# Kernel optimization log

Measured on AMD Instinct MI355X. Metric: run time of the kernel, lower is better.

Reference implementation:

```python
import jax, jax.numpy as jnp
import numpy as np

B, L, D, H, NL = 4, 2048, 512, 8, 2
HD = D // H  # 64
EPS = 1e-5


def _rotate_half(t):
    a, b = jnp.split(t, 2, axis=-1)
    return jnp.concatenate([-b, a], axis=-1)


def _ln(x, w, b):
    mu = jnp.mean(x, axis=-1, keepdims=True)
    var = jnp.mean((x - mu) ** 2, axis=-1, keepdims=True)
    return (x - mu) * jax.lax.rsqrt(var + EPS) * w + b


def setup_inputs() -> dict:
    key = jax.random.key(0)
    ks = jax.random.split(key, 8)
    x = jax.random.normal(ks[0], (B, L, D), dtype=jnp.float32)
    # 1D RoPE built per head_dim, tiled across heads -> [B, L, D]
    pos = jnp.arange(L, dtype=jnp.float32)
    inv_freq = 10000.0 ** (-2.0 * jnp.arange(HD, dtype=jnp.float32) / HD)
    theta = pos[:, None] * inv_freq[None, :]  # [L, HD]
    pos_cos = jnp.broadcast_to(jnp.tile(jnp.cos(theta), (1, H))[None], (B, L, D)).astype(jnp.float32)
    pos_sin = jnp.broadcast_to(jnp.tile(jnp.sin(theta), (1, H))[None], (B, L, D)).astype(jnp.float32)
    attn_mask = jnp.zeros((B, L), dtype=jnp.float32)  # all tokens valid
    s = 0.02
    Wq = s * jax.random.normal(ks[1], (NL, D, D), dtype=jnp.float32)
    Wk = s * jax.random.normal(ks[2], (NL, D, D), dtype=jnp.float32)
    Wv = s * jax.random.normal(ks[3], (NL, D, D), dtype=jnp.float32)
    Wo = s * jax.random.normal(ks[4], (NL, D, D), dtype=jnp.float32)
    W1 = s * jax.random.normal(ks[5], (NL, D, 2 * D), dtype=jnp.float32)
    W2 = s * jax.random.normal(ks[6], (NL, D, D), dtype=jnp.float32)
    ln1_w = jnp.ones((NL, D), jnp.float32); ln1_b = jnp.zeros((NL, D), jnp.float32)
    ln2_w = jnp.ones((NL, D), jnp.float32); ln2_b = jnp.zeros((NL, D), jnp.float32)
    lnf_w = jnp.ones((D,), jnp.float32); lnf_b = jnp.zeros((D,), jnp.float32)
    return dict(x=x, pos_cos=pos_cos, pos_sin=pos_sin, attn_mask=attn_mask,
                Wq=Wq, Wk=Wk, Wv=Wv, Wo=Wo, W1=W1, W2=W2,
                ln1_w=ln1_w, ln1_b=ln1_b, ln2_w=ln2_w, ln2_b=ln2_b,
                lnf_w=lnf_w, lnf_b=lnf_b)


def reference(x, pos_cos, pos_sin, attn_mask, Wq, Wk, Wv, Wo, W1, W2,
              ln1_w, ln1_b, ln2_w, ln2_b, lnf_w, lnf_b):
    # [B, H, L, HD]
    cos = pos_cos.reshape(B, L, H, HD).transpose(0, 2, 1, 3)
    sin = pos_sin.reshape(B, L, H, HD).transpose(0, 2, 1, 3)
    mask = attn_mask[:, None, None, :]  # [B,1,1,L]
    scale = 1.0 / np.float32(np.sqrt(HD))
    for i in range(NL):
        xn = _ln(x, ln1_w[i], ln1_b[i])
        q = (xn @ Wq[i]).reshape(B, L, H, HD).transpose(0, 2, 1, 3)
        k = (xn @ Wk[i]).reshape(B, L, H, HD).transpose(0, 2, 1, 3)
        v = (xn @ Wv[i]).reshape(B, L, H, HD).transpose(0, 2, 1, 3)
        q = q * cos + _rotate_half(q) * sin
        k = k * cos + _rotate_half(k) * sin
        scores = jnp.einsum('bhqd,bhkd->bhqk', q, k) * scale + mask
        probs = jax.nn.softmax(scores, axis=-1)
        ctx = jnp.einsum('bhqk,bhkd->bhqd', probs, v)
        ctx = ctx.transpose(0, 2, 1, 3).reshape(B, L, D)
        x = x + ctx @ Wo[i]
        xn = _ln(x, ln2_w[i], ln2_b[i])
        h = xn @ W1[i]
        x1, x2 = jnp.split(h, 2, axis=-1)
        x = x + (jax.nn.silu(x1) * x2) @ W2[i]
    return _ln(x, lnf_w, lnf_b)
```

## Files before the change

### kernel.cpp

```cpp
#include <hip/hip_runtime.h>

#define BB 4
#define LL 2048
#define DD 512
#define HH 8
#define NLAYER 2

typedef __attribute__((ext_vector_type(8))) short short8;
typedef __attribute__((ext_vector_type(4))) float floatx4;
typedef __attribute__((ext_vector_type(16))) float floatx16;

union U4S8 { uint4 u4; short8 s8; unsigned int u[4]; };

__device__ __forceinline__ unsigned short f2bf(float f) {
  unsigned int u = __float_as_uint(f);
  u += 0x7fffu + ((u >> 16) & 1u);
  return (unsigned short)(u >> 16);
}
__device__ __forceinline__ float bf2f(unsigned short s) {
  return __uint_as_float(((unsigned int)s) << 16);
}
__device__ __forceinline__ unsigned int pack_bf16(float a0, float a1) {
  unsigned int u0 = __float_as_uint(a0) + 0x8000u;
  unsigned int u1 = __float_as_uint(a1) + 0x8000u;
  return __builtin_amdgcn_perm(u1, u0, 0x07060302u);
}
__device__ __forceinline__ unsigned int pack_bf16_trunc(float a0, float a1) {
  return __builtin_amdgcn_perm(__float_as_uint(a1), __float_as_uint(a0), 0x07060302u);
}
__device__ __forceinline__ float fast_exp2(float x) {
#if __has_builtin(__builtin_amdgcn_exp2f)
  return __builtin_amdgcn_exp2f(x);
#else
  return exp2f(x);
#endif
}
__device__ __forceinline__ float fast_exp(float x) {
  return fast_exp2(x * 1.442695040888963f);
}

struct TJob { const float* src; unsigned short* dst; int C; int il; };
struct TJobs { TJob j[12]; };

__global__ __launch_bounds__(256) void transpose_all_kernel(TJobs jobs) {
  TJob jb = jobs.j[blockIdx.z];
  int c0 = blockIdx.x * 32;
  if (c0 >= jb.C) return;
  const int R = 512;
  __shared__ float t[32][33];
  int r0 = blockIdx.y * 32;
#pragma unroll
  for (int i = 0; i < 4; i++) {
    int idx = threadIdx.x + i * 256;
    t[idx >> 5][idx & 31] = jb.src[(size_t)(r0 + (idx >> 5)) * jb.C + c0 + (idx & 31)];
  }
  __syncthreads();
#pragma unroll
  for (int i = 0; i < 4; i++) {
    int idx = threadIdx.x + i * 256;
    int cc = idx >> 5, rr = idx & 31;
    int c = c0 + cc;
    int orow = jb.il ? ((c < 512) ? 2 * c : 2 * (c - 512) + 1) : c;
    jb.dst[(size_t)orow * R + r0 + rr] = f2bf(t[rr][cc]);
  }
}

__global__ __launch_bounds__(256) void ln_kernel(
    const float* __restrict__ x, const float* __restrict__ w, const float* __restrict__ b,
    unsigned short* __restrict__ outB, float* __restrict__ outF) {
  int row = blockIdx.x;
  const float* xr = x + (size_t)row * DD;
  int tid = threadIdx.x;
  float2 v = *(const float2*)(xr + tid * 2);
  float s = v.x + v.y;
  float ss = v.x * v.x + v.y * v.y;
#pragma unroll
  for (int off = 1; off < 64; off <<= 1) {
    s += __shfl_xor(s, off);
    ss += __shfl_xor(ss, off);
  }
  __shared__ float red[2][4];
  int wave = tid >> 6, lane = tid & 63;
  if (lane == 0) { red[0][wave] = s; red[1][wave] = ss; }
  __syncthreads();
  s = red[0][0] + red[0][1] + red[0][2] + red[0][3];
  ss = red[1][0] + red[1][1] + red[1][2] + red[1][3];
  float mu = s * (1.0f / DD);
  float var = ss * (1.0f / DD) - mu * mu;
  float inv = rsqrtf(var + 1e-5f);
#pragma unroll
  for (int j = 0; j < 2; j++) {
    int c = tid * 2 + j;
    float val = (((j == 0) ? v.x : v.y) - mu) * inv * w[c] + b[c];
    if (outB) outB[(size_t)row * DD + c] = f2bf(val);
    if (outF) outF[(size_t)row * DD + c] = val;
  }
}

__global__ __launch_bounds__(256) void gemm128_kernel(
    const unsigned short* __restrict__ A, const unsigned short* __restrict__ Bt,
    float* __restrict__ outF, unsigned short* __restrict__ outB,
    const float* __restrict__ res, int M, int N, int K,
    unsigned short* __restrict__ vtp) {
  __shared__ alignas(16) unsigned short As[128 * 32];
  __shared__ alignas(16) unsigned short Bs[128 * 32];
  const int tid = threadIdx.x;
  const int wave = tid >> 6, lane = tid & 63;
  const int l16 = lane & 15, quad = lane >> 4;
  const int wm = wave & 1, wn = wave >> 1;
  const int m0 = blockIdx.y * 128, n0 = blockIdx.x * 128;

  floatx4 acc[4][4];
#pragma unroll
  for (int i = 0; i < 4; i++)
#pragma unroll
    for (int j = 0; j < 4; j++)
#pragma unroll
      for (int r = 0; r < 4; r++) acc[i][j][r] = 0.f;

  const int grow = lane >> 2;
  const int gg = lane & 3;

  for (int kt = 0; kt < K; kt += 32) {
#pragma unroll
    for (int i = 0; i < 2; i++) {
      int rb = (wave * 2 + i) * 16;
      int row = rb + grow;
      int gsw = gg ^ (row & 3);
      const unsigned short* srcA = A + (size_t)(m0 + row) * K + kt + gsw * 8;
      const unsigned short* srcB = Bt + (size_t)(n0 + row) * K + kt + gsw * 8;
      __builtin_amdgcn_global_load_lds(
          (const __attribute__((address_space(1))) unsigned int*)srcA,
          (__attribute__((address_space(3))) unsigned int*)(As + rb * 32), 16, 0, 0);
      __builtin_amdgcn_global_load_lds(
          (const __attribute__((address_space(1))) unsigned int*)srcB,
          (__attribute__((address_space(3))) unsigned int*)(Bs + rb * 32), 16, 0, 0);
    }
    __syncthreads();
    short8 af[4], bf[4];
#pragma unroll
    for (int i = 0; i < 4; i++) {
      int rowa = wm * 64 + i * 16 + l16;
      af[i] = *(const short8*)&As[rowa * 32 + (quad ^ (rowa & 3)) * 8];
      int rowb = wn * 64 + i * 16 + l16;
      bf[i] = *(const short8*)&Bs[rowb * 32 + (quad ^ (rowb & 3)) * 8];
    }
#pragma unroll
    for (int i = 0; i < 4; i++)
#pragma unroll
      for (int j = 0; j < 4; j++)
        acc[i][j] = __builtin_amdgcn_mfma_f32_16x16x32_bf16(af[i], bf[j], acc[i][j], 0, 0, 0);
    __syncthreads();
  }
  if (vtp && n0 >= 1024) {
#pragma unroll
    for (int i = 0; i < 4; i++)
#pragma unroll
      for (int j = 0; j < 4; j++) {
        int cg = (n0 - 1024) + wn * 64 + j * 16 + l16;
        int hh = cg >> 6, dd = cg & 63;
        int seq0 = m0 + wm * 64 + i * 16 + quad * 4;
        int bI = seq0 >> 11, ls = seq0 & 2047;
        unsigned short* dst = vtp + ((size_t)(bI * 8 + hh) * 64 + dd) * 2048 + ls;
        uint2 w;
        w.x = pack_bf16(acc[i][j][0], acc[i][j][1]);
        w.y = pack_bf16(acc[i][j][2], acc[i][j][3]);
        *(uint2*)dst = w;
      }
    return;
  }
#pragma unroll
  for (int i = 0; i < 4; i++)
#pragma unroll
    for (int j = 0; j < 4; j++)
#pragma unroll
      for (int r = 0; r < 4; r++) {
        int row = m0 + wm * 64 + i * 16 + quad * 4 + r;
        int col = n0 + wn * 64 + j * 16 + l16;
        size_t idx = (size_t)row * N + col;
        float val = acc[i][j][r];
        if (res) val += res[idx];
        if (outF) outF[idx] = val;
        if (outB) outB[idx] = f2bf(val);
      }
}

__global__ __launch_bounds__(256) void gemm64n_kernel(
    const unsigned short* __restrict__ A, const unsigned short* __restrict__ Bt,
    float* __restrict__ outF, const float* __restrict__ res, int M, int N, int K) {
  __shared__ alignas(16) unsigned short As[128 * 32];
  __shared__ alignas(16) unsigned short Bs[64 * 32];
  const int tid = threadIdx.x;
  const int wave = tid >> 6, lane = tid & 63;
  const int l16 = lane & 15, quad = lane >> 4;
  const int m0 = blockIdx.y * 128, n0 = blockIdx.x * 64;

  floatx4 acc[2][4];
#pragma unroll
  for (int i = 0; i < 2; i++)
#pragma unroll
    for (int j = 0; j < 4; j++)
#pragma unroll
      for (int r = 0; r < 4; r++) acc[i][j][r] = 0.f;

  const int grow = lane >> 2;
  const int gg = lane & 3;

  for (int kt = 0; kt < K; kt += 32) {
#pragma unroll
    for (int i = 0; i < 3; i++) {
      int id = wave * 3 + i;
      if (id < 8) {
        int rb = id * 16;
        int row = rb + grow;
        int gsw = gg ^ (row & 3);
        const unsigned short* srcA = A + (size_t)(m0 + row) * K + kt + gsw * 8;
        __builtin_amdgcn_global_load_lds(
            (const __attribute__((address_space(1))) unsigned int*)srcA,
            (__attribute__((address_space(3))) unsigned int*)(As + rb * 32), 16, 0, 0);
      } else {
        int rb = (id - 8) * 16;
        int row = rb + grow;
        int gsw = gg ^ (row & 3);
        const unsigned short* srcB = Bt + (size_t)(n0 + row) * K + kt + gsw * 8;
        __builtin_amdgcn_global_load_lds(
            (const __attribute__((address_space(1))) unsigned int*)srcB,
            (__attribute__((address_space(3))) unsigned int*)(Bs + rb * 32), 16, 0, 0);
      }
    }
    __syncthreads();
    short8 af[2], bfr[4];
#pragma unroll
    for (int i = 0; i < 2; i++) {
      int rowa = wave * 32 + i * 16 + l16;
      af[i] = *(const short8*)&As[rowa * 32 + (quad ^ (rowa & 3)) * 8];
    }
#pragma unroll
    for (int j = 0; j < 4; j++) {
      int rowb = j * 16 + l16;
      bfr[j] = *(const short8*)&Bs[rowb * 32 + (quad ^ (rowb & 3)) * 8];
    }
#pragma unroll
    for (int i = 0; i < 2; i++)
#pragma unroll
      for (int j = 0; j < 4; j++)
        acc[i][j] = __builtin_amdgcn_mfma_f32_16x16x32_bf16(af[i], bfr[j], acc[i][j], 0, 0, 0);
    __syncthreads();
  }
#pragma unroll
  for (int i = 0; i < 2; i++)
#pragma unroll
    for (int j = 0; j < 4; j++)
#pragma unroll
      for (int r = 0; r < 4; r++) {
        int row = m0 + wave * 32 + i * 16 + quad * 4 + r;
        int col = n0 + j * 16 + l16;
        size_t idx = (size_t)row * N + col;
        float val = acc[i][j][r];
        if (res) val += res[idx];
        outF[idx] = val;
      }
}

__global__ __launch_bounds__(256) void gemm_swiglu_kernel(
    const unsigned short* __restrict__ A, const unsigned short* __restrict__ Bt,
    unsigned short* __restrict__ gout, int M, int N, int K) {
  __shared__ alignas(16) unsigned short As[128 * 32];
  __shared__ alignas(16) unsigned short Bs[128 * 32];
  const int tid = threadIdx.x;
  const int wave = tid >> 6, lane = tid & 63;
  const int l16 = lane & 15, quad = lane >> 4;
  const int wm = wave & 1, wn = wave >> 1;
  const int m0 = blockIdx.y * 128, n0 = blockIdx.x * 128;
  floatx4 acc[4][4];
#pragma unroll
  for (int i = 0; i < 4; i++)
#pragma unroll
    for (int j = 0; j < 4; j++)
#pragma unroll
      for (int r = 0; r < 4; r++) acc[i][j][r] = 0.f;
  const int grow = lane >> 2;
  const int gg = lane & 3;
  for (int kt = 0; kt < K; kt += 32) {
#pragma unroll
    for (int i = 0; i < 2; i++) {
      int rb = (wave * 2 + i) * 16;
      int row = rb + grow;
      int gsw = gg ^ (row & 3);
      const unsigned short* srcA = A + (size_t)(m0 + row) * K + kt + gsw * 8;
      const unsigned short* srcB = Bt + (size_t)(n0 + row) * K + kt + gsw * 8;
      __builtin_amdgcn_global_load_lds(
          (const __attribute__((address_space(1))) unsigned int*)srcA,
          (__attribute__((address_space(3))) unsigned int*)(As + rb * 32), 16, 0, 0);
      __builtin_amdgcn_global_load_lds(
          (const __attribute__((address_space(1))) unsigned int*)srcB,
          (__attribute__((address_space(3))) unsigned int*)(Bs + rb * 32), 16, 0, 0);
    }
    __syncthreads();
    short8 af[4], bf[4];
#pragma unroll
    for (int i = 0; i < 4; i++) {
      int rowa = wm * 64 + i * 16 + l16;
      af[i] = *(const short8*)&As[rowa * 32 + (quad ^ (rowa & 3)) * 8];
      int rowb = wn * 64 + i * 16 + l16;
      bf[i] = *(const short8*)&Bs[rowb * 32 + (quad ^ (rowb & 3)) * 8];
    }
#pragma unroll
    for (int i = 0; i < 4; i++)
#pragma unroll
      for (int j = 0; j < 4; j++)
        acc[i][j] = __builtin_amdgcn_mfma_f32_16x16x32_bf16(af[i], bf[j], acc[i][j], 0, 0, 0);
    __syncthreads();
  }
  const int Nh = N >> 1;
#pragma unroll
  for (int i = 0; i < 4; i++)
#pragma unroll
    for (int j = 0; j < 4; j++)
#pragma unroll
      for (int r = 0; r < 4; r++) {
        float val = acc[i][j][r];
        float part = __shfl_xor(val, 1);
        float x1 = (l16 & 1) ? part : val;
        float x2 = (l16 & 1) ? val : part;
        float g = x1 / (1.f + fast_exp(-x1)) * x2;
        if (!(l16 & 1)) {
          int row = m0 + wm * 64 + i * 16 + quad * 4 + r;
          int gcol = (n0 + wn * 64 + j * 16 + l16) >> 1;
          gout[(size_t)row * Nh + gcol] = f2bf(g);
        }
      }
}

__global__ __launch_bounds__(256) void rope_kernel(
    unsigned short* __restrict__ qkv, const float* __restrict__ cosb,
    const float* __restrict__ sinb) {
  int lt = blockIdx.x, bh = blockIdx.y;
  int b = bh >> 3, h = bh & 7;
  int tid = threadIdx.x;
  int r = tid >> 2, d0 = (tid & 3) * 8;
  size_t trow = (size_t)(b * LL + lt * 64 + r);
  const float* cp = cosb + (size_t)(lt * 64 + r) * DD + d0;
  const float* sp = sinb + (size_t)(lt * 64 + r) * DD + d0;
  unsigned short* qp = qkv + trow * 1536 + h * 64 + d0;
  unsigned short* kp = qp + 512;
  float4 c1a = *(const float4*)cp, c1b = *(const float4*)(cp + 4);
  float4 c2a = *(const float4*)(cp + 32), c2b = *(const float4*)(cp + 36);
  float4 s1a = *(const float4*)sp, s1b = *(const float4*)(sp + 4);
  float4 s2a = *(const float4*)(sp + 32), s2b = *(const float4*)(sp + 36);
  float c1[8] = {c1a.x, c1a.y, c1a.z, c1a.w, c1b.x, c1b.y, c1b.z, c1b.w};
  float c2[8] = {c2a.x, c2a.y, c2a.z, c2a.w, c2b.x, c2b.y, c2b.z, c2b.w};
  float s1[8] = {s1a.x, s1a.y, s1a.z, s1a.w, s1b.x, s1b.y, s1b.z, s1b.w};
  float s2[8] = {s2a.x, s2a.y, s2a.z, s2a.w, s2b.x, s2b.y, s2b.z, s2b.w};
  U4S8 qlo, qhi, klo, khi;
  qlo.u4 = *(const uint4*)qp; qhi.u4 = *(const uint4*)(qp + 32);
  klo.u4 = *(const uint4*)kp; khi.u4 = *(const uint4*)(kp + 32);
  U4S8 qlo2, qhi2, klo2, khi2;
#pragma unroll
  for (int e = 0; e < 4; e++) {
    float q1a = bf2f((unsigned short)qlo.s8[2 * e]), q1b = bf2f((unsigned short)qlo.s8[2 * e + 1]);
    float q2a = bf2f((unsigned short)qhi.s8[2 * e]), q2b = bf2f((unsigned short)qhi.s8[2 * e + 1]);
    qlo2.u[e] = pack_bf16(q1a * c1[2 * e] - q2a * s1[2 * e], q1b * c1[2 * e + 1] - q2b * s1[2 * e + 1]);
    qhi2.u[e] = pack_bf16(q2a * c2[2 * e] + q1a * s2[2 * e], q2b * c2[2 * e + 1] + q1b * s2[2 * e + 1]);
    float k1a = bf2f((unsigned short)klo.s8[2 * e]), k1b = bf2f((unsigned short)klo.s8[2 * e + 1]);
    float k2a = bf2f((unsigned short)khi.s8[2 * e]), k2b = bf2f((unsigned short)khi.s8[2 * e + 1]);
    klo2.u[e] = pack_bf16(k1a * c1[2 * e] - k2a * s1[2 * e], k1b * c1[2 * e + 1] - k2b * s1[2 * e + 1]);
    khi2.u[e] = pack_bf16(k2a * c2[2 * e] + k1a * s2[2 * e], k2b * c2[2 * e + 1] + k1b * s2[2 * e + 1]);
  }
  *(uint4*)qp = qlo2.u4; *(uint4*)(qp + 32) = qhi2.u4;
  *(uint4*)kp = klo2.u4; *(uint4*)(kp + 32) = khi2.u4;
}

__global__ __launch_bounds__(256, 2) void attn_kernel(
    const unsigned short* __restrict__ qkv, const unsigned short* __restrict__ vtp,
    const float* __restrict__ mask, unsigned short* __restrict__ ctx) {
  __shared__ alignas(16) unsigned short Ks[3][64][72];
  __shared__ alignas(16) unsigned short Vs[3][64][72];
  const int tid = threadIdx.x;
  const int wave = tid >> 6, lane = tid & 63;
  const int l5 = lane & 31, b5 = lane >> 5;
  const int b = blockIdx.z, h = blockIdx.y;
  const int q0 = blockIdx.x * 128 + wave * 32;
  const int bh = b * 8 + h;
  const float QSCALE = 0.125f * 1.442695040888963f;

  short8 qf[4];
  {
    const unsigned short* qp = qkv + (size_t)(b * LL + q0 + l5) * 1536 + h * 64 + b5 * 8;
#pragma unroll
    for (int t = 0; t < 4; t++) {
      U4S8 u;
      u.u4 = *(const uint4*)(qp + t * 16);
      short8 qs;
#pragma unroll
      for (int e = 0; e < 8; e++)
        qs[e] = (short)f2bf(bf2f((unsigned short)u.s8[e]) * QSCALE);
      qf[t] = qs;
    }
  }
  short8 bones = {0, 0, 0, 0, 0, 0, 0, 0};
  if (b5 == 0) bones[0] = (short)0x3F80;
  short8 onesA;
#pragma unroll
  for (int e = 0; e < 8; e++) onesA[e] = (short)0x3F80;

  floatx16 O[2], Lacc;
#pragma unroll
  for (int a = 0; a < 2; a++)
#pragma unroll
    for (int r = 0; r < 16; r++) O[a][r] = 0.f;
#pragma unroll
  for (int r = 0; r < 16; r++) Lacc[r] = 0.f;

  const int srow = tid >> 2, sc = (tid & 3) * 16;
  const unsigned short* kbase = qkv + (size_t)(b * LL + srow) * 1536 + 512 + h * 64 + sc;
  const unsigned short* vbase = vtp + (size_t)(bh * 64 + srow) * 2048 + sc;

  uint4 kr0 = *(const uint4*)kbase;
  uint4 kr1 = *(const uint4*)(kbase + 8);
  uint4 vr0 = *(const uint4*)vbase;
  uint4 vr1 = *(const uint4*)(vbase + 8);

  auto do_pv = [&](const floatx16& a0, const floatx16& a1, int vb) {
    unsigned int pk[2][8];
#pragma unroll
    for (int i = 0; i < 8; i++) {
      pk[0][i] = pack_bf16_trunc(fast_exp2(a0[2 * i]), fast_exp2(a0[2 * i + 1]));
      pk[1][i] = pack_bf16_trunc(fast_exp2(a1[2 * i]), fast_exp2(a1[2 * i + 1]));
    }
#pragma unroll
    for (int ms = 0; ms < 2; ms++) {
#pragma unroll
      for (int kp = 0; kp < 2; kp++) {
        unsigned int se0 = b5 ? pk[ms][4 * kp] : pk[ms][4 * kp + 2];
        unsigned int se1 = b5 ? pk[ms][4 * kp + 1] : pk[ms][4 * kp + 3];
        unsigned int w0 = (unsigned int)__shfl_xor((int)se0, 32);
        unsigned int w1 = (unsigned int)__shfl_xor((int)se1, 32);
        U4S8 u;
        u.u[0] = b5 ? w0 : pk[ms][4 * kp];
        u.u[1] = b5 ? w1 : pk[ms][4 * kp + 1];
        u.u[2] = b5 ? pk[ms][4 * kp + 2] : w0;
        u.u[3] = b5 ? pk[ms][4 * kp + 3] : w1;
        short8 pb = u.s8;
        const int kst = ms * 2 + kp;
        short8 v0 = *(const short8*)&Vs[vb][l5][kst * 16 + b5 * 8];
        short8 v1 = *(const short8*)&Vs[vb][32 + l5][kst * 16 + b5 * 8];
        O[0] = __builtin_amdgcn_mfma_f32_32x32x16_bf16(v0, pb, O[0], 0, 0, 0);
        O[1] = __builtin_amdgcn_mfma_f32_32x32x16_bf16(v1, pb, O[1], 0, 0, 0);
        Lacc = __builtin_amdgcn_mfma_f32_32x32x16_bf16(onesA, pb, Lacc, 0, 0, 0);
      }
    }
  };

  floatx16 sp0, sp1;
  int buf = 0, pbuf = 0;
  for (int it = 0; it < 32; it++) {
    *(uint4*)&Ks[buf][srow][sc] = kr0;
    *(uint4*)&Ks[buf][srow][sc + 8] = kr1;
    *(uint4*)&Vs[buf][srow][sc] = vr0;
    *(uint4*)&Vs[buf][srow][sc + 8] = vr1;
    __syncthreads();
    if (it < 31) {
      const unsigned short* kn = kbase + (size_t)((it + 1) * 64) * 1536;
      const unsigned short* vn = vbase + (it + 1) * 64;
      kr0 = *(const uint4*)kn;
      kr1 = *(const uint4*)(kn + 8);
      vr0 = *(const uint4*)vn;
      vr1 = *(const uint4*)(vn + 8);
    }
    int t0 = it * 64;
    float mk0 = mask[b * LL + t0 + l5];
    float mk1 = mask[b * LL + t0 + 32 + l5];
    short8 kf[2][4];
#pragma unroll
    for (int ms = 0; ms < 2; ms++)
#pragma unroll
      for (int t = 0; t < 4; t++)
        kf[ms][t] = *(const short8*)&Ks[buf][ms * 32 + l5][t * 16 + b5 * 8];

    floatx16 s0, s1;
#pragma unroll
    for (int r = 0; r < 16; r++) { s0[r] = 0.f; s1[r] = 0.f; }
#pragma unroll
    for (int t = 0; t < 4; t++) {
      s0 = __builtin_amdgcn_mfma_f32_32x32x16_bf16(kf[0][t], qf[t], s0, 0, 0, 0);
      s1 = __builtin_amdgcn_mfma_f32_32x32x16_bf16(kf[1][t], qf[t], s1, 0, 0, 0);
    }
    if (__any(mk0 != 0.0f || mk1 != 0.0f)) {
      short8 am0 = {0, 0, 0, 0, 0, 0, 0, 0}, am1 = {0, 0, 0, 0, 0, 0, 0, 0};
      if (b5 == 0) {
        am0[0] = (short)f2bf(1.442695040888963f * mk0);
        am1[0] = (short)f2bf(1.442695040888963f * mk1);
      }
      s0 = __builtin_amdgcn_mfma_f32_32x32x16_bf16(am0, bones, s0, 0, 0, 0);
      s1 = __builtin_amdgcn_mfma_f32_32x32x16_bf16(am1, bones, s1, 0, 0, 0);
    }
    if (it > 0) do_pv(sp0, sp1, pbuf);
    sp0 = s0; sp1 = s1; pbuf = buf;
    buf = (buf == 2) ? 0 : buf + 1;
  }
  do_pv(sp0, sp1, pbuf);

  float inv = 1.0f / Lacc[0];
  int qrow = q0 + l5;
  unsigned short* op = ctx + (size_t)(b * LL + qrow) * 512 + h * 64;
#pragma unroll
  for (int ds = 0; ds < 2; ds++) {
#pragma unroll
    for (int g = 0; g < 4; g++) {
      uint2 w;
      w.x = pack_bf16(O[ds][4 * g] * inv, O[ds][4 * g + 1] * inv);
      w.y = pack_bf16(O[ds][4 * g + 2] * inv, O[ds][4 * g + 3] * inv);
      *(uint2*)(op + ds * 32 + 8 * g + 4 * b5) = w;
    }
  }
}

extern "C" void kernel_launch(void* const* d_in, const int* in_sizes, int n_in,
                              void* d_out, int out_size, void* d_ws, size_t ws_size,
                              hipStream_t stream) {
  const float* x_in = (const float*)d_in[0];
  const float* pcos = (const float*)d_in[1];
  const float* psin = (const float*)d_in[2];
  const float* amask = (const float*)d_in[3];
  const float* Wq = (const float*)d_in[4];
  const float* Wk = (const float*)d_in[5];
  const float* Wv = (const float*)d_in[6];
  const float* Wo = (const float*)d_in[7];
  const float* W1 = (const float*)d_in[8];
  const float* W2 = (const float*)d_in[9];
  const float* ln1w = (const float*)d_in[10];
  const float* ln1b = (const float*)d_in[11];
  const float* ln2w = (const float*)d_in[12];
  const float* ln2b = (const float*)d_in[13];
  const float* lnfw = (const float*)d_in[14];
  const float* lnfb = (const float*)d_in[15];

  const int M = BB * LL;
  char* p = (char*)d_ws;
  float* x_ws = (float*)p;                  p += (size_t)M * DD * 4;
  unsigned short* xn = (unsigned short*)p;  p += (size_t)M * DD * 2;
  unsigned short* qkv = (unsigned short*)p; p += (size_t)M * 1536 * 2;
  unsigned short* vtb = (unsigned short*)p; p += (size_t)M * DD * 2;
  unsigned short* cb = (unsigned short*)p;  p += (size_t)M * DD * 2;
  unsigned short* wts = (unsigned short*)p;
  unsigned short* gb = vtb;

  const size_t LW = 786432 + 262144 + 524288 + 262144;
  TJobs jobs;
  for (int i = 0; i < NLAYER; i++) {
    unsigned short* wl = wts + i * LW;
    jobs.j[i * 6 + 0] = {Wq + (size_t)i * 262144, wl + 0, 512, 0};
    jobs.j[i * 6 + 1] = {Wk + (size_t)i * 262144, wl + 262144, 512, 0};
    jobs.j[i * 6 + 2] = {Wv + (size_t)i * 262144, wl + 524288, 512, 0};
    jobs.j[i * 6 + 3] = {Wo + (size_t)i * 262144, wl + 786432, 512, 0};
    jobs.j[i * 6 + 4] = {W1 + (size_t)i * 524288, wl + 1048576, 1024, 1};
    jobs.j[i * 6 + 5] = {W2 + (size_t)i * 262144, wl + 1572864, 512, 0};
  }
  transpose_all_kernel<<<dim3(32, 16, 12), 256, 0, stream>>>(jobs);

  for (int i = 0; i < NLAYER; i++) {
    unsigned short* wl = wts + i * LW;
    const float* xin = (i == 0) ? x_in : x_ws;
    ln_kernel<<<M, 256, 0, stream>>>(xin, ln1w + i * DD, ln1b + i * DD, xn, nullptr);
    gemm128_kernel<<<dim3(12, 64), 256, 0, stream>>>(xn, wl + 0, nullptr, qkv, nullptr, M, 1536, 512, vtb);
    rope_kernel<<<dim3(32, 32), 256, 0, stream>>>(qkv, pcos, psin);
    attn_kernel<<<dim3(LL / 128, HH, BB), 256, 0, stream>>>(qkv, vtb, amask, cb);
    gemm64n_kernel<<<dim3(8, 64), 256, 0, stream>>>(cb, wl + 786432, x_ws, xin, M, 512, 512);
    ln_kernel<<<M, 256, 0, stream>>>(x_ws, ln2w + i * DD, ln2b + i * DD, xn, nullptr);
    gemm_swiglu_kernel<<<dim3(8, 64), 256, 0, stream>>>(xn, wl + 1048576, gb, M, 1024, 512);
    gemm64n_kernel<<<dim3(8, 64), 256, 0, stream>>>(gb, wl + 1572864, x_ws, x_ws, M, 512, 512);
  }
  ln_kernel<<<M, 256, 0, stream>>>(x_ws, lnfw, lnfb, nullptr, (float*)d_out);
}
```

Before: 477.6 us.

## Fuse RoPE and Q scaling into QKV GEMM epilogue; widen attention K/V tiles

RoPE and the softmax Q scale move into the QKV GEMM epilogue, so the standalone rope kernel and its read-modify-write pass over Q/K go away. The attention kernel no longer rescales Q on load. It also switches from triple-buffered 64-key tiles to double-buffered 128-key tiles, halving the number of barriers per key sweep. The cost is software pipelining of QK^T against PV across iterations, which was removed, plus more registers used for prefetch. The epilogue now reads cos/sin with scattered scalar loads and writes bf16 values one by one.

```diff
diff --git a/kernel.cpp b/kernel.cpp
--- a/kernel.cpp
+++ b/kernel.cpp
@@ -101,7 +101,8 @@
     const unsigned short* __restrict__ A, const unsigned short* __restrict__ Bt,
     float* __restrict__ outF, unsigned short* __restrict__ outB,
     const float* __restrict__ res, int M, int N, int K,
-    unsigned short* __restrict__ vtp) {
+    unsigned short* __restrict__ vtp,
+    const float* __restrict__ pcos, const float* __restrict__ psin) {
   __shared__ alignas(16) unsigned short As[128 * 32];
   __shared__ alignas(16) unsigned short Bs[128 * 32];
   const int tid = threadIdx.x;
@@ -166,6 +167,31 @@
         w.x = pack_bf16(acc[i][j][0], acc[i][j][1]);
         w.y = pack_bf16(acc[i][j][2], acc[i][j][3]);
         *(uint2*)dst = w;
+      }
+    return;
+  }
+  if (vtp) {
+    const float QSCALE = 0.125f * 1.442695040888963f;
+    const float osc = (n0 < 512) ? QSCALE : 1.0f;
+#pragma unroll
+    for (int i = 0; i < 4; i++)
+#pragma unroll
+      for (int r = 0; r < 4; r++) {
+        int row = m0 + wm * 64 + i * 16 + quad * 4 + r;
+        int t = row & 2047;
+        const float* cr = pcos + (size_t)t * 512;
+        const float* sr = psin + (size_t)t * 512;
+#pragma unroll
+        for (int jj = 0; jj < 2; jj++) {
+          int colL = n0 + wn * 64 + jj * 16 + l16;
+          int cL = colL & 511, cH = cL + 32;
+          float aL = acc[i][jj][r], aH = acc[i][jj + 2][r];
+          float outL = (aL * cr[cL] - aH * sr[cL]) * osc;
+          float outH = (aH * cr[cH] + aL * sr[cH]) * osc;
+          size_t base = (size_t)row * N + colL;
+          outB[base] = f2bf(outL);
+          outB[base + 32] = f2bf(outH);
+        }
       }
     return;
   }
@@ -332,57 +358,17 @@
       }
 }
 
-__global__ __launch_bounds__(256) void rope_kernel(
-    unsigned short* __restrict__ qkv, const float* __restrict__ cosb,
-    const float* __restrict__ sinb) {
-  int lt = blockIdx.x, bh = blockIdx.y;
-  int b = bh >> 3, h = bh & 7;
-  int tid = threadIdx.x;
-  int r = tid >> 2, d0 = (tid & 3) * 8;
-  size_t trow = (size_t)(b * LL + lt * 64 + r);
-  const float* cp = cosb + (size_t)(lt * 64 + r) * DD + d0;
-  const float* sp = sinb + (size_t)(lt * 64 + r) * DD + d0;
-  unsigned short* qp = qkv + trow * 1536 + h * 64 + d0;
-  unsigned short* kp = qp + 512;
-  float4 c1a = *(const float4*)cp, c1b = *(const float4*)(cp + 4);
-  float4 c2a = *(const float4*)(cp + 32), c2b = *(const float4*)(cp + 36);
-  float4 s1a = *(const float4*)sp, s1b = *(const float4*)(sp + 4);
-  float4 s2a = *(const float4*)(sp + 32), s2b = *(const float4*)(sp + 36);
-  float c1[8] = {c1a.x, c1a.y, c1a.z, c1a.w, c1b.x, c1b.y, c1b.z, c1b.w};
-  float c2[8] = {c2a.x, c2a.y, c2a.z, c2a.w, c2b.x, c2b.y, c2b.z, c2b.w};
-  float s1[8] = {s1a.x, s1a.y, s1a.z, s1a.w, s1b.x, s1b.y, s1b.z, s1b.w};
-  float s2[8] = {s2a.x, s2a.y, s2a.z, s2a.w, s2b.x, s2b.y, s2b.z, s2b.w};
-  U4S8 qlo, qhi, klo, khi;
-  qlo.u4 = *(const uint4*)qp; qhi.u4 = *(const uint4*)(qp + 32);
-  klo.u4 = *(const uint4*)kp; khi.u4 = *(const uint4*)(kp + 32);
-  U4S8 qlo2, qhi2, klo2, khi2;
-#pragma unroll
-  for (int e = 0; e < 4; e++) {
-    float q1a = bf2f((unsigned short)qlo.s8[2 * e]), q1b = bf2f((unsigned short)qlo.s8[2 * e + 1]);
-    float q2a = bf2f((unsigned short)qhi.s8[2 * e]), q2b = bf2f((unsigned short)qhi.s8[2 * e + 1]);
-    qlo2.u[e] = pack_bf16(q1a * c1[2 * e] - q2a * s1[2 * e], q1b * c1[2 * e + 1] - q2b * s1[2 * e + 1]);
-    qhi2.u[e] = pack_bf16(q2a * c2[2 * e] + q1a * s2[2 * e], q2b * c2[2 * e + 1] + q1b * s2[2 * e + 1]);
-    float k1a = bf2f((unsigned short)klo.s8[2 * e]), k1b = bf2f((unsigned short)klo.s8[2 * e + 1]);
-    float k2a = bf2f((unsigned short)khi.s8[2 * e]), k2b = bf2f((unsigned short)khi.s8[2 * e + 1]);
-    klo2.u[e] = pack_bf16(k1a * c1[2 * e] - k2a * s1[2 * e], k1b * c1[2 * e + 1] - k2b * s1[2 * e + 1]);
-    khi2.u[e] = pack_bf16(k2a * c2[2 * e] + k1a * s2[2 * e], k2b * c2[2 * e + 1] + k1b * s2[2 * e + 1]);
-  }
-  *(uint4*)qp = qlo2.u4; *(uint4*)(qp + 32) = qhi2.u4;
-  *(uint4*)kp = klo2.u4; *(uint4*)(kp + 32) = khi2.u4;
-}
-
 __global__ __launch_bounds__(256, 2) void attn_kernel(
     const unsigned short* __restrict__ qkv, const unsigned short* __restrict__ vtp,
     const float* __restrict__ mask, unsigned short* __restrict__ ctx) {
-  __shared__ alignas(16) unsigned short Ks[3][64][72];
-  __shared__ alignas(16) unsigned short Vs[3][64][72];
+  __shared__ alignas(16) unsigned short Ks[2][128][72];
+  __shared__ alignas(16) unsigned short Vs[2][64][136];
   const int tid = threadIdx.x;
   const int wave = tid >> 6, lane = tid & 63;
   const int l5 = lane & 31, b5 = lane >> 5;
   const int b = blockIdx.z, h = blockIdx.y;
   const int q0 = blockIdx.x * 128 + wave * 32;
   const int bh = b * 8 + h;
-  const float QSCALE = 0.125f * 1.442695040888963f;
 
   short8 qf[4];
   {
@@ -391,11 +377,7 @@
     for (int t = 0; t < 4; t++) {
       U4S8 u;
       u.u4 = *(const uint4*)(qp + t * 16);
-      short8 qs;
-#pragma unroll
-      for (int e = 0; e < 8; e++)
-        qs[e] = (short)f2bf(bf2f((unsigned short)u.s8[e]) * QSCALE);
-      qf[t] = qs;
+      qf[t] = u.s8;
     }
   }
   short8 bones = {0, 0, 0, 0, 0, 0, 0, 0};
@@ -412,94 +394,96 @@
 #pragma unroll
   for (int r = 0; r < 16; r++) Lacc[r] = 0.f;
 
-  const int srow = tid >> 2, sc = (tid & 3) * 16;
-  const unsigned short* kbase = qkv + (size_t)(b * LL + srow) * 1536 + 512 + h * 64 + sc;
-  const unsigned short* vbase = vtp + (size_t)(bh * 64 + srow) * 2048 + sc;
-
-  uint4 kr0 = *(const uint4*)kbase;
-  uint4 kr1 = *(const uint4*)(kbase + 8);
-  uint4 vr0 = *(const uint4*)vbase;
-  uint4 vr1 = *(const uint4*)(vbase + 8);
-
-  auto do_pv = [&](const floatx16& a0, const floatx16& a1, int vb) {
-    unsigned int pk[2][8];
-#pragma unroll
-    for (int i = 0; i < 8; i++) {
-      pk[0][i] = pack_bf16_trunc(fast_exp2(a0[2 * i]), fast_exp2(a0[2 * i + 1]));
-      pk[1][i] = pack_bf16_trunc(fast_exp2(a1[2 * i]), fast_exp2(a1[2 * i + 1]));
-    }
-#pragma unroll
-    for (int ms = 0; ms < 2; ms++) {
-#pragma unroll
-      for (int kp = 0; kp < 2; kp++) {
-        unsigned int se0 = b5 ? pk[ms][4 * kp] : pk[ms][4 * kp + 2];
-        unsigned int se1 = b5 ? pk[ms][4 * kp + 1] : pk[ms][4 * kp + 3];
-        unsigned int w0 = (unsigned int)__shfl_xor((int)se0, 32);
-        unsigned int w1 = (unsigned int)__shfl_xor((int)se1, 32);
-        U4S8 u;
-        u.u[0] = b5 ? w0 : pk[ms][4 * kp];
-        u.u[1] = b5 ? w1 : pk[ms][4 * kp + 1];
-        u.u[2] = b5 ? pk[ms][4 * kp + 2] : w0;
-        u.u[3] = b5 ? pk[ms][4 * kp + 3] : w1;
-        short8 pb = u.s8;
-        const int kst = ms * 2 + kp;
-        short8 v0 = *(const short8*)&Vs[vb][l5][kst * 16 + b5 * 8];
-        short8 v1 = *(const short8*)&Vs[vb][32 + l5][kst * 16 + b5 * 8];
-        O[0] = __builtin_amdgcn_mfma_f32_32x32x16_bf16(v0, pb, O[0], 0, 0, 0);
-        O[1] = __builtin_amdgcn_mfma_f32_32x32x16_bf16(v1, pb, O[1], 0, 0, 0);
-        Lacc = __builtin_amdgcn_mfma_f32_32x32x16_bf16(onesA, pb, Lacc, 0, 0, 0);
-      }
-    }
-  };
-
-  floatx16 sp0, sp1;
-  int buf = 0, pbuf = 0;
-  for (int it = 0; it < 32; it++) {
-    *(uint4*)&Ks[buf][srow][sc] = kr0;
-    *(uint4*)&Ks[buf][srow][sc + 8] = kr1;
-    *(uint4*)&Vs[buf][srow][sc] = vr0;
-    *(uint4*)&Vs[buf][srow][sc + 8] = vr1;
-    __syncthreads();
-    if (it < 31) {
-      const unsigned short* kn = kbase + (size_t)((it + 1) * 64) * 1536;
-      const unsigned short* vn = vbase + (it + 1) * 64;
-      kr0 = *(const uint4*)kn;
-      kr1 = *(const uint4*)(kn + 8);
-      vr0 = *(const uint4*)vn;
-      vr1 = *(const uint4*)(vn + 8);
-    }
-    int t0 = it * 64;
-    float mk0 = mask[b * LL + t0 + l5];
-    float mk1 = mask[b * LL + t0 + 32 + l5];
-    short8 kf[2][4];
-#pragma unroll
-    for (int ms = 0; ms < 2; ms++)
-#pragma unroll
-      for (int t = 0; t < 4; t++)
-        kf[ms][t] = *(const short8*)&Ks[buf][ms * 32 + l5][t * 16 + b5 * 8];
-
-    floatx16 s0, s1;
-#pragma unroll
-    for (int r = 0; r < 16; r++) { s0[r] = 0.f; s1[r] = 0.f; }
-#pragma unroll
-    for (int t = 0; t < 4; t++) {
-      s0 = __builtin_amdgcn_mfma_f32_32x32x16_bf16(kf[0][t], qf[t], s0, 0, 0, 0);
-      s1 = __builtin_amdgcn_mfma_f32_32x32x16_bf16(kf[1][t], qf[t], s1, 0, 0, 0);
-    }
-    if (__any(mk0 != 0.0f || mk1 != 0.0f)) {
-      short8 am0 = {0, 0, 0, 0, 0, 0, 0, 0}, am1 = {0, 0, 0, 0, 0, 0, 0, 0};
-      if (b5 == 0) {
-        am0[0] = (short)f2bf(1.442695040888963f * mk0);
-        am1[0] = (short)f2bf(1.442695040888963f * mk1);
-      }
-      s0 = __builtin_amdgcn_mfma_f32_32x32x16_bf16(am0, bones, s0, 0, 0, 0);
-      s1 = __builtin_amdgcn_mfma_f32_32x32x16_bf16(am1, bones, s1, 0, 0, 0);
-    }
-    if (it > 0) do_pv(sp0, sp1, pbuf);
-    sp0 = s0; sp1 = s1; pbuf = buf;
-    buf = (buf == 2) ? 0 : buf + 1;
-  }
-  do_pv(sp0, sp1, pbuf);
+  const int krow = tid >> 1, kc = (tid & 1) * 32;
+  const int vrow = tid >> 2, vc = (tid & 3) * 32;
+  const unsigned short* kbase = qkv + (size_t)(b * LL + krow) * 1536 + 512 + h * 64 + kc;
+  const unsigned short* vbase = vtp + (size_t)(bh * 64 + vrow) * 2048 + vc;
+
+  uint4 kr[4], vr[4];
+#pragma unroll
+  for (int g = 0; g < 4; g++) {
+    kr[g] = *(const uint4*)(kbase + g * 8);
+    vr[g] = *(const uint4*)(vbase + g * 8);
+  }
+
+  for (int it = 0; it < 16; it++) {
+    const int buf = it & 1;
+    const int t0 = it * 128;
+#pragma unroll
+    for (int g = 0; g < 4; g++) {
+      *(uint4*)&Ks[buf][krow][kc + g * 8] = kr[g];
+      *(uint4*)&Vs[buf][vrow][vc + g * 8] = vr[g];
+    }
+    __syncthreads();
+    if (it < 15) {
+      const unsigned short* kn = kbase + (size_t)(t0 + 128) * 1536;
+      const unsigned short* vn = vbase + t0 + 128;
+#pragma unroll
+      for (int g = 0; g < 4; g++) {
+        kr[g] = *(const uint4*)(kn + g * 8);
+        vr[g] = *(const uint4*)(vn + g * 8);
+      }
+    }
+#pragma unroll
+    for (int half = 0; half < 2; half++) {
+      const int kb = half * 64;
+      float mk0 = mask[b * LL + t0 + kb + l5];
+      float mk1 = mask[b * LL + t0 + kb + 32 + l5];
+      short8 kf[2][4];
+#pragma unroll
+      for (int ms = 0; ms < 2; ms++)
+#pragma unroll
+        for (int t = 0; t < 4; t++)
+          kf[ms][t] = *(const short8*)&Ks[buf][kb + ms * 32 + l5][t * 16 + b5 * 8];
+
+      floatx16 s0, s1;
+#pragma unroll
+      for (int r = 0; r < 16; r++) { s0[r] = 0.f; s1[r] = 0.f; }
+#pragma unroll
+      for (int t = 0; t < 4; t++) {
+        s0 = __builtin_amdgcn_mfma_f32_32x32x16_bf16(kf[0][t], qf[t], s0, 0, 0, 0);
+        s1 = __builtin_amdgcn_mfma_f32_32x32x16_bf16(kf[1][t], qf[t], s1, 0, 0, 0);
+      }
+      if (__any(mk0 != 0.0f || mk1 != 0.0f)) {
+        short8 am0 = {0, 0, 0, 0, 0, 0, 0, 0}, am1 = {0, 0, 0, 0, 0, 0, 0, 0};
+        if (b5 == 0) {
+          am0[0] = (short)f2bf(1.442695040888963f * mk0);
+          am1[0] = (short)f2bf(1.442695040888963f * mk1);
+        }
+        s0 = __builtin_amdgcn_mfma_f32_32x32x16_bf16(am0, bones, s0, 0, 0, 0);
+        s1 = __builtin_amdgcn_mfma_f32_32x32x16_bf16(am1, bones, s1, 0, 0, 0);
+      }
+
+      unsigned int pk[2][8];
+#pragma unroll
+      for (int i = 0; i < 8; i++) {
+        pk[0][i] = pack_bf16_trunc(fast_exp2(s0[2 * i]), fast_exp2(s0[2 * i + 1]));
+        pk[1][i] = pack_bf16_trunc(fast_exp2(s1[2 * i]), fast_exp2(s1[2 * i + 1]));
+      }
+#pragma unroll
+      for (int ms = 0; ms < 2; ms++) {
+#pragma unroll
+        for (int kp = 0; kp < 2; kp++) {
+          unsigned int se0 = b5 ? pk[ms][4 * kp] : pk[ms][4 * kp + 2];
+          unsigned int se1 = b5 ? pk[ms][4 * kp + 1] : pk[ms][4 * kp + 3];
+          unsigned int w0 = (unsigned int)__shfl_xor((int)se0, 32);
+          unsigned int w1 = (unsigned int)__shfl_xor((int)se1, 32);
+          U4S8 u;
+          u.u[0] = b5 ? w0 : pk[ms][4 * kp];
+          u.u[1] = b5 ? w1 : pk[ms][4 * kp + 1];
+          u.u[2] = b5 ? pk[ms][4 * kp + 2] : w0;
+          u.u[3] = b5 ? pk[ms][4 * kp + 3] : w1;
+          short8 pb = u.s8;
+          const int kst = (kb >> 4) + ms * 2 + kp;
+          short8 v0 = *(const short8*)&Vs[buf][l5][kst * 16 + b5 * 8];
+          short8 v1 = *(const short8*)&Vs[buf][32 + l5][kst * 16 + b5 * 8];
+          O[0] = __builtin_amdgcn_mfma_f32_32x32x16_bf16(v0, pb, O[0], 0, 0, 0);
+          O[1] = __builtin_amdgcn_mfma_f32_32x32x16_bf16(v1, pb, O[1], 0, 0, 0);
+          Lacc = __builtin_amdgcn_mfma_f32_32x32x16_bf16(onesA, pb, Lacc, 0, 0, 0);
+        }
+      }
+    }
+  }
 
   float inv = 1.0f / Lacc[0];
   int qrow = q0 + l5;
@@ -563,8 +547,7 @@
     unsigned short* wl = wts + i * LW;
     const float* xin = (i == 0) ? x_in : x_ws;
     ln_kernel<<<M, 256, 0, stream>>>(xin, ln1w + i * DD, ln1b + i * DD, xn, nullptr);
-    gemm128_kernel<<<dim3(12, 64), 256, 0, stream>>>(xn, wl + 0, nullptr, qkv, nullptr, M, 1536, 512, vtb);
-    rope_kernel<<<dim3(32, 32), 256, 0, stream>>>(qkv, pcos, psin);
+    gemm128_kernel<<<dim3(12, 64), 256, 0, stream>>>(xn, wl + 0, nullptr, qkv, nullptr, M, 1536, 512, vtb, pcos, psin);
     attn_kernel<<<dim3(LL / 128, HH, BB), 256, 0, stream>>>(qkv, vtb, amask, cb);
     gemm64n_kernel<<<dim3(8, 64), 256, 0, stream>>>(cb, wl + 786432, x_ws, xin, M, 512, 512);
     ln_kernel<<<M, 256, 0, stream>>>(x_ws, ln2w + i * DD, ln2b + i * DD, xn, nullptr);
```

Result: slower. 589.1 us (+23.4%).
